# Kernel tuning notes

Measured on AMD Instinct MI355X. Metric: run time of the kernel, lower is better.

Reference implementation:

```python
import jax, jax.numpy as jnp
import numpy as np
import math

BS, SEQ, HID = 1, 2048, 2048
NH, NKV, HD = 32, 8, 64
BASE = 10000.0


def rotate_half(x):
    x1, x2 = x[..., : x.shape[-1] // 2], x[..., x.shape[-1] // 2 :]
    return jnp.concatenate((-x2, x1), axis=-1)


def setup_inputs() -> dict:
    key = jax.random.key(0)
    ks = jax.random.split(key, 6)
    s = 0.02
    return {
        "x": jax.random.normal(ks[0], (BS, SEQ, HID), dtype=jnp.float32),
        "attention_mask": jnp.zeros((BS, SEQ), dtype=jnp.float32),
        "position_ids": jnp.broadcast_to(jnp.arange(SEQ, dtype=jnp.int64 if jax.config.jax_enable_x64 else jnp.int32), (BS, SEQ)),
        "wq": jax.random.normal(ks[1], (HID, NH * HD), dtype=jnp.float32) * s,
        "wk": jax.random.normal(ks[2], (HID, NKV * HD), dtype=jnp.float32) * s,
        "wv": jax.random.normal(ks[3], (HID, NKV * HD), dtype=jnp.float32) * s,
        "wo": jax.random.normal(ks[4], (NH * HD, HID), dtype=jnp.float32) * s,
    }


def reference(x, attention_mask, position_ids, wq, wk, wv, wo):
    bs, seq, _ = x.shape
    groups = NH // NKV

    q = (x @ wq).reshape(bs, seq, NH, HD).transpose(0, 2, 1, 3)   # [b,H,S,D]
    k = (x @ wk).reshape(bs, seq, NKV, HD).transpose(0, 2, 1, 3)  # [b,Hkv,S,D]
    v = (x @ wv).reshape(bs, seq, NKV, HD).transpose(0, 2, 1, 3)

    # rotary embedding
    inv_freq = 1.0 / (BASE ** (jnp.arange(0, HD, 2, dtype=jnp.float32) / HD))  # [D/2]
    freqs = position_ids.astype(jnp.float32)[:, :, None] * inv_freq[None, None, :]  # [b,S,D/2]
    emb = jnp.concatenate((freqs, freqs), axis=-1)               # [b,S,D]
    cos = jnp.cos(emb)[:, None, :, :].astype(x.dtype)            # [b,1,S,D]
    sin = jnp.sin(emb)[:, None, :, :].astype(x.dtype)
    q = q * cos + rotate_half(q) * sin
    k = k * cos + rotate_half(k) * sin

    # repeat_kv (GQA expand)
    k = jnp.repeat(k, groups, axis=1)  # [b,H,S,D]
    v = jnp.repeat(v, groups, axis=1)

    scores = jnp.einsum("bhqd,bhkd->bhqk", q, k) / math.sqrt(HD)
    scores = scores + attention_mask[:, None, None, :]
    attn = jax.nn.softmax(scores.astype(jnp.float32), axis=-1).astype(q.dtype)
    out = jnp.einsum("bhqk,bhkd->bhqd", attn, v)                 # [b,H,S,D]
    out = out.transpose(0, 2, 1, 3).reshape(bs, seq, NH * HD)
    return out @ wo
```

## Files before the change

### kernel.cpp

```cpp
#include <hip/hip_runtime.h>

#define SEQ 2048
#define HID 2048
#define NH  32
#define NKV 8
#define HD  64

typedef _Float16 f16;
typedef __attribute__((ext_vector_type(4))) _Float16 f16x4;
typedef __attribute__((ext_vector_type(8))) _Float16 f16x8;
typedef __attribute__((ext_vector_type(2))) __fp16   h16x2;
typedef __attribute__((ext_vector_type(4))) float    f32x4;

__device__ __forceinline__ f32x4 mfma_16x16x32(f16x8 a, f16x8 b, f32x4 c) {
    return __builtin_amdgcn_mfma_f32_16x16x32_f16(a, b, c, 0, 0, 0);
}

__device__ __forceinline__ void async16(const void* g, void* l) {
    __builtin_amdgcn_global_load_lds(
        (const __attribute__((address_space(1))) void*)g,
        (__attribute__((address_space(3))) void*)l,
        16, 0, 0);
}

__global__ void prep_all(const float* __restrict__ x,
                         const float* __restrict__ wq, const float* __restrict__ wk,
                         const float* __restrict__ wv, const float* __restrict__ wo,
                         f16* __restrict__ xb,
                         f16* __restrict__ Wcat, f16* __restrict__ woT) {
    __shared__ float tile[32][33];
    int z = blockIdx.z;
    int tx = threadIdx.x, ty = threadIdx.y;
    if (z == 4) {
        int idx = (blockIdx.y * 64 + blockIdx.x) * 256 + ty * 32 + tx;
        int i = idx * 4;
        float4 v = *(const float4*)(x + i);
        f16x4 o = { (f16)v.x, (f16)v.y, (f16)v.z, (f16)v.w };
        *(f16x4*)(xb + i) = o;
        return;
    }
    const float* src; f16* dst; int C;
    if      (z == 0) { src = wq; dst = Wcat;                         C = 2048; }
    else if (z == 1) { src = wk; dst = Wcat + (size_t)2048 * 2048;   C = 512;  }
    else if (z == 2) { src = wv; dst = Wcat + (size_t)2560 * 2048;   C = 512;  }
    else             { src = wo; dst = woT;                          C = 2048; }
    int c0 = blockIdx.x * 32, r0 = blockIdx.y * 32;
    if (c0 >= C) return;
#pragma unroll
    for (int i = 0; i < 32; i += 8)
        tile[ty + i][tx] = src[(size_t)(r0 + ty + i) * C + c0 + tx];
    __syncthreads();
#pragma unroll
    for (int i = 0; i < 32; i += 8)
        dst[(size_t)(c0 + ty + i) * 2048 + r0 + tx] = (f16)tile[tx][ty + i];
}

template <int MODE>
__global__ __launch_bounds__(256)
void gemm_bt(const f16* __restrict__ A, const f16* __restrict__ BT,
             float* __restrict__ Cf, f16* __restrict__ Q, f16* __restrict__ Kk,
             f16* __restrict__ VT, const int* __restrict__ pos,
             const float* __restrict__ mask, int N, int K) {
    __shared__ f16 As[2][64 * 64];
    __shared__ f16 Bs[2][128 * 64];
    int t = threadIdx.x;
    int w = t >> 6, lane = t & 63, quad = lane >> 4, l15 = lane & 15;
    int wm = w >> 1, wn = w & 1;
    int m0 = blockIdx.y * 64, n0 = blockIdx.x * 128;
    int sw = l15 & 7;

    int r8 = lane >> 3;
    int cc = (lane & 7) ^ r8;
    const f16* Ag0 = A  + (size_t)(m0 + w * 16 + r8) * K + cc * 8;
    const f16* Ag1 = Ag0 + (size_t)8 * K;
    const f16* Bg  = BT + (size_t)(n0 + w * 32 + r8) * K + cc * 8;

    f32x4 acc[2][4] = {};

    async16(Ag0, &As[0][w * 1024]);
    async16(Ag1, &As[0][w * 1024 + 512]);
#pragma unroll
    for (int g = 0; g < 4; g++)
        async16(Bg + (size_t)(8 * g) * K, &Bs[0][w * 2048 + g * 512]);
    __syncthreads();

    int b = 0;
    for (int kt = 64; kt <= K; kt += 64) {
        if (kt < K) {
            async16(Ag0 + kt, &As[b ^ 1][w * 1024]);
            async16(Ag1 + kt, &As[b ^ 1][w * 1024 + 512]);
#pragma unroll
            for (int g = 0; g < 4; g++)
                async16(Bg + (size_t)(8 * g) * K + kt, &Bs[b ^ 1][w * 2048 + g * 512]);
        }
        f16x8 af[2][2], bf[4][2];
#pragma unroll
        for (int mi = 0; mi < 2; mi++) {
            int row = wm * 32 + mi * 16 + l15;
#pragma unroll
            for (int kh = 0; kh < 2; kh++)
                af[mi][kh] = *(const f16x8*)(&As[b][row * 64 + ((kh * 4 + quad) ^ sw) * 8]);
        }
#pragma unroll
        for (int ni = 0; ni < 4; ni++) {
            int row = wn * 64 + ni * 16 + l15;
#pragma unroll
            for (int kh = 0; kh < 2; kh++)
                bf[ni][kh] = *(const f16x8*)(&Bs[b][row * 64 + ((kh * 4 + quad) ^ sw) * 8]);
        }
#pragma unroll
        for (int mi = 0; mi < 2; mi++)
#pragma unroll
            for (int ni = 0; ni < 4; ni++) {
                acc[mi][ni] = mfma_16x16x32(af[mi][0], bf[ni][0], acc[mi][ni]);
                acc[mi][ni] = mfma_16x16x32(af[mi][1], bf[ni][1], acc[mi][ni]);
            }
        __syncthreads();
        b ^= 1;
    }

    int rb  = m0 + wm * 32 + quad * 4;
    int cbh = n0 + wn * 64;
    if (MODE == 0) {
        if (cbh < (NH + NKV) * HD) {
            bool isQ = cbh < NH * HD;
            f16* dst = isQ ? (Q  + (size_t)(cbh >> 6) * SEQ * HD)
                           : (Kk + (size_t)((cbh - NH * HD) >> 6) * SEQ * HD);
            float scale = isQ ? 0.18033688011112042f : 1.0f;
            float fr[2];
#pragma unroll
            for (int ni = 0; ni < 2; ni++)
                fr[ni] = __builtin_amdgcn_exp2f(
                    (float)(ni * 16 + l15) * -0.41524101186092029f);
#pragma unroll
            for (int mi = 0; mi < 2; mi++)
#pragma unroll
                for (int r = 0; r < 4; r++) {
                    int row = rb + mi * 16 + r;
                    float pv = (float)pos[row];
#pragma unroll
                    for (int ni = 0; ni < 2; ni++) {
                        float sn, cs;
                        __sincosf(pv * fr[ni], &sn, &cs);
                        float x1 = acc[mi][ni][r], x2 = acc[mi][ni + 2][r];
                        int d = ni * 16 + l15;
                        dst[(size_t)row * HD + d]      = (f16)(scale * (x1 * cs - x2 * sn));
                        dst[(size_t)row * HD + d + 32] = (f16)(scale * (x2 * cs + x1 * sn));
                    }
                }
        } else {
            const float LOG2E = 1.4426950408889634f;
#pragma unroll
            for (int mi = 0; mi < 2; mi++) {
                float4 mv = *(const float4*)(mask + rb + mi * 16);
                float em[4];
#pragma unroll
                for (int r = 0; r < 4; r++)
                    em[r] = __builtin_amdgcn_exp2f((&mv.x)[r] * LOG2E);
#pragma unroll
                for (int ni = 0; ni < 4; ni++) {
                    int c2 = cbh - (NH + NKV) * HD + ni * 16 + l15;
                    f16x4 v4;
                    ((h16x2*)&v4)[0] = __builtin_amdgcn_cvt_pkrtz(
                        acc[mi][ni][0] * em[0], acc[mi][ni][1] * em[1]);
                    ((h16x2*)&v4)[1] = __builtin_amdgcn_cvt_pkrtz(
                        acc[mi][ni][2] * em[2], acc[mi][ni][3] * em[3]);
                    *(f16x4*)(VT + (size_t)c2 * SEQ + rb + mi * 16) = v4;
                }
            }
        }
    } else {
#pragma unroll
        for (int mi = 0; mi < 2; mi++)
#pragma unroll
            for (int ni = 0; ni < 4; ni++)
#pragma unroll
                for (int r = 0; r < 4; r++)
                    Cf[(size_t)(rb + mi * 16 + r) * N + cbh + ni * 16 + l15] =
                        acc[mi][ni][r];
    }
}

__global__ __launch_bounds__(512)
void attn_fused(const f16* __restrict__ Qb, const f16* __restrict__ Kb,
                const f16* __restrict__ VTb, const float* __restrict__ mask,
                f16* __restrict__ Opart, float* __restrict__ Lpart) {
    __shared__ f16 Ks[2][64 * 64];
    __shared__ f16 Vs[2][64 * 64];
    __shared__ f16 Em[SEQ / 2];

    int t = threadIdx.x, w = t >> 6, lane = t & 63, quad = lane >> 4, l15 = lane & 15;
    int h = blockIdx.y, kvh = h >> 2, split = blockIdx.z;
    int qbase = blockIdx.x * 256 + w * 32;
    int key0  = split * (SEQ / 2);
    const f16* Qh = Qb  + (size_t)h   * SEQ * HD;
    const f16* Kh = Kb  + (size_t)kvh * SEQ * HD;
    const f16* Vh = VTb + (size_t)kvh * HD * SEQ;
    int sw = l15 & 7;
    const float LOG2E = 1.4426950408889634f;

    if (t < 128) {
        int idx = t * 8;
        float4 ma = *(const float4*)(mask + key0 + idx);
        float4 mb = *(const float4*)(mask + key0 + idx + 4);
        f16x8 e;
        ((h16x2*)&e)[0] = __builtin_amdgcn_cvt_pkrtz(
            __builtin_amdgcn_exp2f(ma.x * LOG2E), __builtin_amdgcn_exp2f(ma.y * LOG2E));
        ((h16x2*)&e)[1] = __builtin_amdgcn_cvt_pkrtz(
            __builtin_amdgcn_exp2f(ma.z * LOG2E), __builtin_amdgcn_exp2f(ma.w * LOG2E));
        ((h16x2*)&e)[2] = __builtin_amdgcn_cvt_pkrtz(
            __builtin_amdgcn_exp2f(mb.x * LOG2E), __builtin_amdgcn_exp2f(mb.y * LOG2E));
        ((h16x2*)&e)[3] = __builtin_amdgcn_cvt_pkrtz(
            __builtin_amdgcn_exp2f(mb.z * LOG2E), __builtin_amdgcn_exp2f(mb.w * LOG2E));
        *(f16x8*)(&Em[idx]) = e;
    }

    int r8 = lane >> 3;
    int cc = (lane & 7) ^ r8;
    bool isK = w < 4;
    int ws = isK ? w : (w - 4);
    const f16* g0;
    long gstep;
    if (isK) {
        int gk = 32 * (ws >> 1) + 4 * (ws & 1) + 8 * (r8 >> 2) + (r8 & 3);
        g0 = Kh + (size_t)(key0 + gk) * HD + cc * 8;
        gstep = (long)16 * HD;
    } else {
        g0 = Vh + (size_t)(ws * 16 + r8) * SEQ + key0 + cc * 8;
        gstep = (long)8 * SEQ;
    }
    const f16* g1 = g0 + gstep;
    long adv = isK ? (long)64 * HD : 64;
    int lr0 = ws * 16 * 64, lr1 = lr0 + 8 * 64;

    {
        f16* dst = isK ? &Ks[0][0] : &Vs[0][0];
        async16(g0, dst + lr0);
        async16(g1, dst + lr1);
    }

    f16x8 bq[2][2];
#pragma unroll
    for (int qg = 0; qg < 2; qg++)
#pragma unroll
        for (int ks = 0; ks < 2; ks++)
            bq[qg][ks] = *(const f16x8*)(Qh + (size_t)(qbase + qg * 16 + l15) * HD
                                            + ks * 32 + quad * 8);

    f32x4 o[4][2] = {};
    f32x4 ol[2]   = {};

    int c0 = (quad ^ sw) * 8, c1 = ((4 | quad) ^ sw) * 8;

    __syncthreads();
    int b = 0;

    for (int ktl = 0; ktl < SEQ / 128; ktl++) {
        if (ktl + 1 < SEQ / 128) {
            g0 += adv; g1 += adv;
            f16* dst = isK ? &Ks[b ^ 1][0] : &Vs[b ^ 1][0];
            async16(g0, dst + lr0);
            async16(g1, dst + lr1);
        }
        const f16* Kb_ = &Ks[b][0];
        const f16* Vb_ = &Vs[b][0];

        f32x4 st[4][2] = {};
#pragma unroll
        for (int ni = 0; ni < 4; ni++) {
            const f16* kr = Kb_ + (ni * 16 + l15) * 64;
            f16x8 ak0 = *(const f16x8*)(kr + c0);
            f16x8 ak1 = *(const f16x8*)(kr + c1);
#pragma unroll
            for (int qg = 0; qg < 2; qg++) {
                st[ni][qg] = mfma_16x16x32(ak0, bq[qg][0], st[ni][qg]);
                st[ni][qg] = mfma_16x16x32(ak1, bq[qg][1], st[ni][qg]);
            }
        }
        f16x8 pb[2][2];
#pragma unroll
        for (int ni = 0; ni < 4; ni++)
#pragma unroll
            for (int qg = 0; qg < 2; qg++) {
                h16x2 lo = __builtin_amdgcn_cvt_pkrtz(
                    __builtin_amdgcn_exp2f(st[ni][qg][0]),
                    __builtin_amdgcn_exp2f(st[ni][qg][1]));
                h16x2 hi = __builtin_amdgcn_cvt_pkrtz(
                    __builtin_amdgcn_exp2f(st[ni][qg][2]),
                    __builtin_amdgcn_exp2f(st[ni][qg][3]));
                ((h16x2*)&pb[qg][ni >> 1])[(ni & 1) * 2]     = lo;
                ((h16x2*)&pb[qg][ni >> 1])[(ni & 1) * 2 + 1] = hi;
            }
        f16x8 em0 = *(const f16x8*)(&Em[ktl * 64 + quad * 8]);
        f16x8 em1 = *(const f16x8*)(&Em[ktl * 64 + 32 + quad * 8]);
#pragma unroll
        for (int qg = 0; qg < 2; qg++) {
            ol[qg] = mfma_16x16x32(em0, pb[qg][0], ol[qg]);
            ol[qg] = mfma_16x16x32(em1, pb[qg][1], ol[qg]);
        }
#pragma unroll
        for (int dt = 0; dt < 4; dt++) {
            const f16* vr = Vb_ + (dt * 16 + l15) * 64;
            f16x8 av0 = *(const f16x8*)(vr + c0);
            f16x8 av1 = *(const f16x8*)(vr + c1);
#pragma unroll
            for (int qg = 0; qg < 2; qg++) {
                o[dt][qg] = mfma_16x16x32(av0, pb[qg][0], o[dt][qg]);
                o[dt][qg] = mfma_16x16x32(av1, pb[qg][1], o[dt][qg]);
            }
        }
        __syncthreads();
        b ^= 1;
    }

    if (quad == 0) {
#pragma unroll
        for (int qg = 0; qg < 2; qg++)
            Lpart[((size_t)split * NH + h) * SEQ + qbase + qg * 16 + l15] =
                ol[qg][0];
    }
    f16* Op = Opart + ((size_t)split * NH + h) * SEQ * HD;
#pragma unroll
    for (int dt = 0; dt < 4; dt++)
#pragma unroll
        for (int qg = 0; qg < 2; qg++) {
            f16x4 v4;
            ((h16x2*)&v4)[0] = __builtin_amdgcn_cvt_pkrtz(o[dt][qg][0], o[dt][qg][1]);
            ((h16x2*)&v4)[1] = __builtin_amdgcn_cvt_pkrtz(o[dt][qg][2], o[dt][qg][3]);
            *(f16x4*)(Op + (size_t)(qbase + qg * 16 + l15) * HD
                         + dt * 16 + quad * 4) = v4;
        }
}

__global__ void attn_combine(const f16* __restrict__ O, const float* __restrict__ L,
                             f16* __restrict__ ctx) {
    int idx = blockIdx.x * 256 + threadIdx.x;
    int c4  = idx & 511;
    int row = idx >> 9;
    int col = c4 * 4;
    int h   = col >> 6;
    float l = L[(size_t)h * SEQ + row] + L[(size_t)(NH + h) * SEQ + row];
    const f16* o0 = O + ((size_t)h * SEQ + row) * HD + (col & 63);
    const f16* o1 = o0 + (size_t)NH * SEQ * HD;
    f16x4 a = *(const f16x4*)o0, b = *(const f16x4*)o1;
    float inv = 1.0f / l;
    f16x4 r;
#pragma unroll
    for (int j = 0; j < 4; j++)
        r[j] = (f16)(((float)a[j] + (float)b[j]) * inv);
    *(f16x4*)(ctx + (size_t)row * (NH * HD) + col) = r;
}

extern "C" void kernel_launch(void* const* d_in, const int* in_sizes, int n_in,
                              void* d_out, int out_size, void* d_ws, size_t ws_size,
                              hipStream_t stream) {
    const float* x    = (const float*)d_in[0];
    const float* mask = (const float*)d_in[1];
    const int*   pos  = (const int*)  d_in[2];
    const float* wq   = (const float*)d_in[3];
    const float* wk   = (const float*)d_in[4];
    const float* wv   = (const float*)d_in[5];
    const float* wo   = (const float*)d_in[6];
    float* out = (float*)d_out;

    char* ws = (char*)d_ws;
    f16*   xb    = (f16*)(ws);
    f16*   Wcat  = (f16*)(ws + ((size_t)8  << 20));
    f16*   woT   = (f16*)(ws + ((size_t)20 << 20));
    f16*   Qb    = (f16*)(ws + ((size_t)28 << 20));
    f16*   Kb    = (f16*)(ws + ((size_t)36 << 20));
    f16*   VTb   = (f16*)(ws + ((size_t)38 << 20));
    f16*   Opart = (f16*)(ws);
    float* Lpart = (float*)(ws + ((size_t)16 << 20));
    f16*   ctx   = (f16*)(ws + ((size_t)28 << 20));

    prep_all<<<dim3(64, 64, 5), dim3(32, 8), 0, stream>>>(
        x, wq, wk, wv, wo, xb, Wcat, woT);

    gemm_bt<0><<<dim3(3072 / 128, 2048 / 64), 256, 0, stream>>>(
        xb, Wcat, nullptr, Qb, Kb, VTb, pos, mask, 3072, 2048);

    attn_fused<<<dim3(SEQ / 256, NH, 2), 512, 0, stream>>>(
        Qb, Kb, VTb, mask, Opart, Lpart);
    attn_combine<<<SEQ * NH * HD / 4 / 256, 256, 0, stream>>>(Opart, Lpart, ctx);

    gemm_bt<1><<<dim3(2048 / 128, 2048 / 64), 256, 0, stream>>>(
        ctx, woT, out, nullptr, nullptr, nullptr, nullptr, nullptr, 2048, 2048);
}
```

Baseline: 208.3 us.

## Drop split-K attention and combine kernel, add XCD remap and finer barriers

Attention no longer splits keys across two blocks. Each block walks the full sequence and normalizes its output in-kernel, writing ctx directly, so the separate combine kernel and its partial-buffer traffic are gone. The per-tile __syncthreads is replaced with explicit vmcnt waits, raw s_barrier and setprio around the MFMA sections. The GEMMs get an XCD-aware block remap to improve L2 locality. In exchange the attention grid halves to 256 blocks, which reduces parallelism on a chip with 256 CUs.

```diff
diff --git a/kernel.cpp b/kernel.cpp
--- a/kernel.cpp
+++ b/kernel.cpp
@@ -21,6 +21,17 @@
         (const __attribute__((address_space(1))) void*)g,
         (__attribute__((address_space(3))) void*)l,
         16, 0, 0);
+}
+
+__device__ __forceinline__ void xcd_colmap(int& bx, int& by) {
+    int gx = gridDim.x, gy = gridDim.y;
+    int nwg = gx * gy;
+    int orig = by * gx + bx;
+    int q = nwg >> 3, r = nwg & 7;
+    int xcd = orig & 7, loc = orig >> 3;
+    int wg = (xcd < r ? xcd * (q + 1) : r * (q + 1) + (xcd - r) * q) + loc;
+    bx = wg / gy;
+    by = wg - bx * gy;
 }
 
 __global__ void prep_all(const float* __restrict__ x,
@@ -66,7 +77,9 @@
     int t = threadIdx.x;
     int w = t >> 6, lane = t & 63, quad = lane >> 4, l15 = lane & 15;
     int wm = w >> 1, wn = w & 1;
-    int m0 = blockIdx.y * 64, n0 = blockIdx.x * 128;
+    int bx = blockIdx.x, by = blockIdx.y;
+    xcd_colmap(bx, by);
+    int m0 = by * 64, n0 = bx * 128;
     int sw = l15 & 7;
 
     int r8 = lane >> 3;
@@ -184,36 +197,19 @@
 __global__ __launch_bounds__(512)
 void attn_fused(const f16* __restrict__ Qb, const f16* __restrict__ Kb,
                 const f16* __restrict__ VTb, const float* __restrict__ mask,
-                f16* __restrict__ Opart, float* __restrict__ Lpart) {
+                f16* __restrict__ ctx) {
     __shared__ f16 Ks[2][64 * 64];
     __shared__ f16 Vs[2][64 * 64];
-    __shared__ f16 Em[SEQ / 2];
+    __shared__ f16 Em[SEQ];
 
     int t = threadIdx.x, w = t >> 6, lane = t & 63, quad = lane >> 4, l15 = lane & 15;
-    int h = blockIdx.y, kvh = h >> 2, split = blockIdx.z;
+    int h = blockIdx.y, kvh = h >> 2;
     int qbase = blockIdx.x * 256 + w * 32;
-    int key0  = split * (SEQ / 2);
     const f16* Qh = Qb  + (size_t)h   * SEQ * HD;
     const f16* Kh = Kb  + (size_t)kvh * SEQ * HD;
     const f16* Vh = VTb + (size_t)kvh * HD * SEQ;
     int sw = l15 & 7;
     const float LOG2E = 1.4426950408889634f;
-
-    if (t < 128) {
-        int idx = t * 8;
-        float4 ma = *(const float4*)(mask + key0 + idx);
-        float4 mb = *(const float4*)(mask + key0 + idx + 4);
-        f16x8 e;
-        ((h16x2*)&e)[0] = __builtin_amdgcn_cvt_pkrtz(
-            __builtin_amdgcn_exp2f(ma.x * LOG2E), __builtin_amdgcn_exp2f(ma.y * LOG2E));
-        ((h16x2*)&e)[1] = __builtin_amdgcn_cvt_pkrtz(
-            __builtin_amdgcn_exp2f(ma.z * LOG2E), __builtin_amdgcn_exp2f(ma.w * LOG2E));
-        ((h16x2*)&e)[2] = __builtin_amdgcn_cvt_pkrtz(
-            __builtin_amdgcn_exp2f(mb.x * LOG2E), __builtin_amdgcn_exp2f(mb.y * LOG2E));
-        ((h16x2*)&e)[3] = __builtin_amdgcn_cvt_pkrtz(
-            __builtin_amdgcn_exp2f(mb.z * LOG2E), __builtin_amdgcn_exp2f(mb.w * LOG2E));
-        *(f16x8*)(&Em[idx]) = e;
-    }
 
     int r8 = lane >> 3;
     int cc = (lane & 7) ^ r8;
@@ -223,10 +219,10 @@
     long gstep;
     if (isK) {
         int gk = 32 * (ws >> 1) + 4 * (ws & 1) + 8 * (r8 >> 2) + (r8 & 3);
-        g0 = Kh + (size_t)(key0 + gk) * HD + cc * 8;
+        g0 = Kh + (size_t)gk * HD + cc * 8;
         gstep = (long)16 * HD;
     } else {
-        g0 = Vh + (size_t)(ws * 16 + r8) * SEQ + key0 + cc * 8;
+        g0 = Vh + (size_t)(ws * 16 + r8) * SEQ + cc * 8;
         gstep = (long)8 * SEQ;
     }
     const f16* g1 = g0 + gstep;
@@ -239,6 +235,16 @@
         async16(g1, dst + lr1);
     }
 
+    {
+        float4 mv = *(const float4*)(mask + t * 4);
+        f16x4 e;
+        ((h16x2*)&e)[0] = __builtin_amdgcn_cvt_pkrtz(
+            __builtin_amdgcn_exp2f(mv.x * LOG2E), __builtin_amdgcn_exp2f(mv.y * LOG2E));
+        ((h16x2*)&e)[1] = __builtin_amdgcn_cvt_pkrtz(
+            __builtin_amdgcn_exp2f(mv.z * LOG2E), __builtin_amdgcn_exp2f(mv.w * LOG2E));
+        *(f16x4*)(&Em[t * 4]) = e;
+    }
+
     f16x8 bq[2][2];
 #pragma unroll
     for (int qg = 0; qg < 2; qg++)
@@ -252,20 +258,28 @@
 
     int c0 = (quad ^ sw) * 8, c1 = ((4 | quad) ^ sw) * 8;
 
-    __syncthreads();
+    asm volatile("s_waitcnt lgkmcnt(0)" ::: "memory");
+
     int b = 0;
-
-    for (int ktl = 0; ktl < SEQ / 128; ktl++) {
-        if (ktl + 1 < SEQ / 128) {
+    const int NT = SEQ / 64;
+    for (int ktl = 0; ktl < NT; ktl++) {
+        if (ktl + 1 < NT) {
             g0 += adv; g1 += adv;
             f16* dst = isK ? &Ks[b ^ 1][0] : &Vs[b ^ 1][0];
             async16(g0, dst + lr0);
             async16(g1, dst + lr1);
-        }
+            asm volatile("s_waitcnt vmcnt(2)" ::: "memory");
+        } else {
+            asm volatile("s_waitcnt vmcnt(0)" ::: "memory");
+        }
+        __builtin_amdgcn_s_barrier();
+        __builtin_amdgcn_sched_barrier(0);
+
         const f16* Kb_ = &Ks[b][0];
         const f16* Vb_ = &Vs[b][0];
 
         f32x4 st[4][2] = {};
+        __builtin_amdgcn_s_setprio(1);
 #pragma unroll
         for (int ni = 0; ni < 4; ni++) {
             const f16* kr = Kb_ + (ni * 16 + l15) * 64;
@@ -277,6 +291,7 @@
                 st[ni][qg] = mfma_16x16x32(ak1, bq[qg][1], st[ni][qg]);
             }
         }
+        __builtin_amdgcn_s_setprio(0);
         f16x8 pb[2][2];
 #pragma unroll
         for (int ni = 0; ni < 4; ni++)
@@ -293,6 +308,7 @@
             }
         f16x8 em0 = *(const f16x8*)(&Em[ktl * 64 + quad * 8]);
         f16x8 em1 = *(const f16x8*)(&Em[ktl * 64 + 32 + quad * 8]);
+        __builtin_amdgcn_s_setprio(1);
 #pragma unroll
         for (int qg = 0; qg < 2; qg++) {
             ol[qg] = mfma_16x16x32(em0, pb[qg][0], ol[qg]);
@@ -309,46 +325,25 @@
                 o[dt][qg] = mfma_16x16x32(av1, pb[qg][1], o[dt][qg]);
             }
         }
-        __syncthreads();
+        __builtin_amdgcn_s_setprio(0);
+        __builtin_amdgcn_sched_barrier(0);
+        __builtin_amdgcn_s_barrier();
         b ^= 1;
     }
 
-    if (quad == 0) {
-#pragma unroll
-        for (int qg = 0; qg < 2; qg++)
-            Lpart[((size_t)split * NH + h) * SEQ + qbase + qg * 16 + l15] =
-                ol[qg][0];
-    }
-    f16* Op = Opart + ((size_t)split * NH + h) * SEQ * HD;
+    float inv[2] = { 1.0f / ol[0][0], 1.0f / ol[1][0] };
 #pragma unroll
     for (int dt = 0; dt < 4; dt++)
 #pragma unroll
         for (int qg = 0; qg < 2; qg++) {
             f16x4 v4;
-            ((h16x2*)&v4)[0] = __builtin_amdgcn_cvt_pkrtz(o[dt][qg][0], o[dt][qg][1]);
-            ((h16x2*)&v4)[1] = __builtin_amdgcn_cvt_pkrtz(o[dt][qg][2], o[dt][qg][3]);
-            *(f16x4*)(Op + (size_t)(qbase + qg * 16 + l15) * HD
-                         + dt * 16 + quad * 4) = v4;
-        }
-}
-
-__global__ void attn_combine(const f16* __restrict__ O, const float* __restrict__ L,
-                             f16* __restrict__ ctx) {
-    int idx = blockIdx.x * 256 + threadIdx.x;
-    int c4  = idx & 511;
-    int row = idx >> 9;
-    int col = c4 * 4;
-    int h   = col >> 6;
-    float l = L[(size_t)h * SEQ + row] + L[(size_t)(NH + h) * SEQ + row];
-    const f16* o0 = O + ((size_t)h * SEQ + row) * HD + (col & 63);
-    const f16* o1 = o0 + (size_t)NH * SEQ * HD;
-    f16x4 a = *(const f16x4*)o0, b = *(const f16x4*)o1;
-    float inv = 1.0f / l;
-    f16x4 r;
-#pragma unroll
-    for (int j = 0; j < 4; j++)
-        r[j] = (f16)(((float)a[j] + (float)b[j]) * inv);
-    *(f16x4*)(ctx + (size_t)row * (NH * HD) + col) = r;
+            ((h16x2*)&v4)[0] = __builtin_amdgcn_cvt_pkrtz(
+                o[dt][qg][0] * inv[qg], o[dt][qg][1] * inv[qg]);
+            ((h16x2*)&v4)[1] = __builtin_amdgcn_cvt_pkrtz(
+                o[dt][qg][2] * inv[qg], o[dt][qg][3] * inv[qg]);
+            *(f16x4*)(ctx + (size_t)(qbase + qg * 16 + l15) * (NH * HD)
+                          + h * HD + dt * 16 + quad * 4) = v4;
+        }
 }
 
 extern "C" void kernel_launch(void* const* d_in, const int* in_sizes, int n_in,
@@ -370,9 +365,7 @@
     f16*   Qb    = (f16*)(ws + ((size_t)28 << 20));
     f16*   Kb    = (f16*)(ws + ((size_t)36 << 20));
     f16*   VTb   = (f16*)(ws + ((size_t)38 << 20));
-    f16*   Opart = (f16*)(ws);
-    float* Lpart = (float*)(ws + ((size_t)16 << 20));
-    f16*   ctx   = (f16*)(ws + ((size_t)28 << 20));
+    f16*   ctx   = (f16*)(ws);
 
     prep_all<<<dim3(64, 64, 5), dim3(32, 8), 0, stream>>>(
         x, wq, wk, wv, wo, xb, Wcat, woT);
@@ -380,9 +373,8 @@
     gemm_bt<0><<<dim3(3072 / 128, 2048 / 64), 256, 0, stream>>>(
         xb, Wcat, nullptr, Qb, Kb, VTb, pos, mask, 3072, 2048);
 
-    attn_fused<<<dim3(SEQ / 256, NH, 2), 512, 0, stream>>>(
-        Qb, Kb, VTb, mask, Opart, Lpart);
-    attn_combine<<<SEQ * NH * HD / 4 / 256, 256, 0, stream>>>(Opart, Lpart, ctx);
+    attn_fused<<<dim3(SEQ / 256, NH), 512, 0, stream>>>(
+        Qb, Kb, VTb, mask, ctx);
 
     gemm_bt<1><<<dim3(2048 / 128, 2048 / 64), 256, 0, stream>>>(
         ctx, woT, out, nullptr, nullptr, nullptr, nullptr, nullptr, 2048, 2048);
```

Measured after the change: 204.6 us. About the same (-1.7%).
